# Kernel optimization log

Hardware: AMD Instinct MI355X
Metric: run time of the kernel (lower is better)

Reference implementation:

```python
import jax, jax.numpy as jnp
import numpy as np

B_SZ, L, D_MODEL = 2, 2048, 1024
EXPAND, N_STATE, K = 2, 16, 4
D_INNER = D_MODEL * EXPAND


def setup_inputs() -> dict:
    key = jax.random.key(0)
    ks = jax.random.split(key, 12)
    s = lambda k, shape, scale=0.02: jax.random.normal(k, shape, jnp.float32) * scale
    return {
        "x": jax.random.normal(ks[0], (B_SZ, L, D_MODEL), jnp.float32),
        "ln_gamma": jnp.ones((D_MODEL,), jnp.float32),
        "ln_beta": jnp.zeros((D_MODEL,), jnp.float32),
        "W_in": s(ks[1], (D_MODEL, 2 * D_INNER)),
        "conv_w": s(ks[2], (D_INNER, 1, K), 0.1),
        "conv_b": jnp.zeros((D_INNER,), jnp.float32),
        "A_log": jax.random.normal(ks[3], (N_STATE,), jnp.float32),
        "B_mat": s(ks[4], (N_STATE, D_INNER), 0.05),
        "C_mat": s(ks[5], (D_INNER, N_STATE), 0.05),
        "D_vec": s(ks[6], (D_INNER,), 0.1),
        "Wd": s(ks[7], (D_INNER, D_INNER)),
        "bd": jnp.zeros((D_INNER,), jnp.float32),
        "W_out": s(ks[8], (D_INNER, D_MODEL)),
    }


def _layernorm(x, g, b, eps=1e-5):
    mu = jnp.mean(x, axis=-1, keepdims=True)
    var = jnp.var(x, axis=-1, keepdims=True)
    return (x - mu) * jax.lax.rsqrt(var + eps) * g + b


def _selective_scan(x, delta, A, B_mat, C_mat, D_vec):
    # x: (b,l,d), delta: (b,l), A: (n,)
    dA = jnp.exp(delta[..., None] * A)            # (b,l,n)
    Bx = jnp.einsum('bld,nd->bln', x, B_mat) * delta[..., None]  # (b,l,n)

    def step(h, inp):
        dA_t, Bx_t = inp
        h = dA_t * h + Bx_t
        return h, h

    h0 = jnp.zeros((x.shape[0], A.shape[0]), x.dtype)
    # scan over seq axis
    _, hs = jax.lax.scan(step, h0, (jnp.swapaxes(dA, 0, 1), jnp.swapaxes(Bx, 0, 1)))
    hs = jnp.swapaxes(hs, 0, 1)                   # (b,l,n)
    return jnp.einsum('bln,dn->bld', hs, C_mat) + D_vec * x


def reference(x, ln_gamma, ln_beta, W_in, conv_w, conv_b, A_log, B_mat, C_mat, D_vec, Wd, bd, W_out):
    residual = x
    h = _layernorm(x, ln_gamma, ln_beta)
    xg = h @ W_in                                  # (b,l,2*d_inner)
    xs, gate = jnp.split(xg, 2, axis=-1)
    # depthwise causal conv (torch pads K-1 both sides then slices [:L] == left pad K-1)
    xc = jnp.swapaxes(xs, 1, 2)                    # (b,d,l)
    xc = jax.lax.conv_general_dilated(
        xc, conv_w, window_strides=(1,), padding=((K - 1, 0),),
        dimension_numbers=('NCH', 'OIH', 'NCH'), feature_group_count=D_INNER)
    xc = xc + conv_b[None, :, None]
    xs = jnp.swapaxes(xc, 1, 2)                    # (b,l,d)
    xs = jax.nn.silu(xs)
    # S4 kernel
    delta = jnp.mean(jax.nn.softplus(xs @ Wd + bd), axis=-1)  # (b,l)
    A = -jnp.exp(A_log)
    y = _selective_scan(xs, delta, A, B_mat, C_mat, D_vec)
    y = y * jax.nn.silu(gate)
    y = y @ W_out
    return residual + y
```

## Files before the change

kernel.cpp:

```cpp
#include <hip/hip_runtime.h>
#include <cstdint>
#include <cstddef>

typedef unsigned short u16;
typedef __attribute__((ext_vector_type(4))) float floatx4;
typedef __attribute__((ext_vector_type(8))) __bf16 bf16x8;

__device__ __forceinline__ float u2f(u16 u) {
    union { unsigned int i; float f; } x;
    x.i = ((unsigned int)u) << 16;
    return x.f;
}
__device__ __forceinline__ u16 f2u(float f) {
    union { float f; unsigned int i; } x;
    x.f = f;
    unsigned int r = x.i + 0x7fffu + ((x.i >> 16) & 1u);
    return (u16)(r >> 16);
}

__device__ __forceinline__ void swz(int bid, int& x, int& y) {
    int xcd = bid & 7;
    int lid = bid >> 3;
    x = lid >> 2;
    y = xcd * 4 + (lid & 3);
}

__device__ __forceinline__ void tr_tile(const float* __restrict__ in, u16* __restrict__ out,
                                        int K, int N, int bx, int by, float* tile ) {
    int n0 = bx * 32, k0 = by * 32;
    int t = threadIdx.x;
    int r = t >> 3, c4 = (t & 7) * 4;
    float4 v = *(const float4*)(in + (size_t)(k0 + r) * N + n0 + c4);
    tile[r * 33 + c4 + 0] = v.x;
    tile[r * 33 + c4 + 1] = v.y;
    tile[r * 33 + c4 + 2] = v.z;
    tile[r * 33 + c4 + 3] = v.w;
    __syncthreads();
    int n = t >> 3, kg = (t & 7) * 4;
    ushort4 o;
    o.x = f2u(tile[(kg + 0) * 33 + n]);
    o.y = f2u(tile[(kg + 1) * 33 + n]);
    o.z = f2u(tile[(kg + 2) * 33 + n]);
    o.w = f2u(tile[(kg + 3) * 33 + n]);
    *(ushort4*)(out + (size_t)(n0 + n) * K + k0 + kg) = o;
}

__global__ __launch_bounds__(256)
void prep_kernel(const float* __restrict__ W_in, u16* __restrict__ Wt_in,
                 const float* __restrict__ Wd, u16* __restrict__ Wt_ext,
                 const float* __restrict__ W_out, u16* __restrict__ Wt_out,
                 const float* __restrict__ B_mat,
                 const float* __restrict__ x, const float* __restrict__ gamma,
                 const float* __restrict__ beta, u16* __restrict__ h,
                 float* __restrict__ out) {
    __shared__ float tile[32 * 33];
    int blk = blockIdx.x, t = threadIdx.x;
    if (blk < 4096) {
        tr_tile(W_in, Wt_in, 1024, 4096, blk & 127, blk >> 7, tile);
    } else if (blk < 8192) {
        int b2 = blk - 4096;
        tr_tile(Wd, Wt_ext, 2048, 2048, b2 & 63, b2 >> 6, tile);
    } else if (blk < 10240) {
        int b3 = blk - 8192;
        tr_tile(W_out, Wt_out, 2048, 1024, b3 & 31, b3 >> 5, tile);
    } else if (blk < 14336) {
        int r = blk - 10240;
        const float4* xr = (const float4*)(x + (size_t)r * 1024);
        float4 xv = xr[t];
        ((float4*)(out + (size_t)r * 1024))[t] = xv;
        float s = xv.x + xv.y + xv.z + xv.w;
        float ss = xv.x * xv.x + xv.y * xv.y + xv.z * xv.z + xv.w * xv.w;
#pragma unroll
        for (int off = 32; off > 0; off >>= 1) {
            s += __shfl_down(s, off, 64);
            ss += __shfl_down(ss, off, 64);
        }
        __shared__ float rs[4], rss[4], mu_s, ri_s;
        int wave = t >> 6, lane = t & 63;
        if (lane == 0) { rs[wave] = s; rss[wave] = ss; }
        __syncthreads();
        if (t == 0) {
            float S = rs[0] + rs[1] + rs[2] + rs[3];
            float SS = rss[0] + rss[1] + rss[2] + rss[3];
            float mu = S * (1.f / 1024.f);
            float var = SS * (1.f / 1024.f) - mu * mu;
            mu_s = mu;
            ri_s = rsqrtf(fmaxf(var, 0.f) + 1e-5f);
        }
        __syncthreads();
        float mu = mu_s, ri = ri_s;
        float4 gv = ((const float4*)gamma)[t];
        float4 bv = ((const float4*)beta)[t];
        ushort4 o;
        o.x = f2u((xv.x - mu) * ri * gv.x + bv.x);
        o.y = f2u((xv.y - mu) * ri * gv.y + bv.y);
        o.z = f2u((xv.z - mu) * ri * gv.z + bv.z);
        o.w = f2u((xv.w - mu) * ri * gv.w + bv.w);
        ((ushort4*)(h + (size_t)r * 1024))[t] = o;
    } else {
        int idx = (blk - 14336) * 256 + t;
        int row = 2048 + (idx >> 11), col = idx & 2047;
        u16 v = (row < 2064) ? f2u(B_mat[(size_t)(row - 2048) * 2048 + col]) : (u16)0;
        Wt_ext[(size_t)row * 2048 + col] = v;
    }
}

__device__ __forceinline__ void gl_lds16(const u16* g, u16* l) {
    __builtin_amdgcn_global_load_lds(
        (const __attribute__((address_space(1))) void*)g,
        (__attribute__((address_space(3))) void*)l, 16, 0, 0);
}

template <int CB, int NB>
__device__ __forceinline__
void ktile256(u16 (&As)[2][16384], u16 (&Bs)[2][16384],
              const u16* __restrict__ gA, const u16* __restrict__ gB,
              int kt, bool doStage, int K,
              int w, int wr, int wc, int l16, int q,
              floatx4 (&acc)[8][4]) {
    asm volatile("s_waitcnt vmcnt(0)" ::: "memory");
    __builtin_amdgcn_s_barrier();
    asm volatile("" ::: "memory");
    bf16x8 af[4][2], bfr[4][2];
    const int aBase = wr * 128, bBase = wc * 64;
#pragma unroll
    for (int i = 0; i < 4; ++i)
#pragma unroll
        for (int h = 0; h < 2; ++h)
            af[i][h] = *(const bf16x8*)&As[CB][h * 8192 + (aBase + i * 16 + l16) * 32 + q * 8];
#pragma unroll
    for (int j = 0; j < 2; ++j)
#pragma unroll
        for (int h = 0; h < 2; ++h)
            bfr[j][h] = *(const bf16x8*)&Bs[CB][h * 8192 + (bBase + j * 16 + l16) * 32 + q * 8];
    if (doStage) {
        const u16* p = gA + (size_t)(kt + 1) * 64;
#pragma unroll
        for (int h = 0; h < 2; ++h) {
            gl_lds16(p + h * 32,                  &As[NB][h * 8192 + w * 1024]);
            gl_lds16(p + (size_t)16 * K + h * 32, &As[NB][h * 8192 + w * 1024 + 512]);
        }
    }
    __builtin_amdgcn_s_barrier();
    __builtin_amdgcn_s_setprio(1);
#pragma unroll
    for (int i = 0; i < 4; ++i)
#pragma unroll
        for (int j = 0; j < 2; ++j)
#pragma unroll
            for (int h = 0; h < 2; ++h)
                acc[i][j] = __builtin_amdgcn_mfma_f32_16x16x32_bf16(af[i][h], bfr[j][h], acc[i][j], 0, 0, 0);
    __builtin_amdgcn_s_setprio(0);
    __builtin_amdgcn_s_barrier();
#pragma unroll
    for (int j = 2; j < 4; ++j)
#pragma unroll
        for (int h = 0; h < 2; ++h)
            bfr[j][h] = *(const bf16x8*)&Bs[CB][h * 8192 + (bBase + j * 16 + l16) * 32 + q * 8];
    if (doStage) {
        const u16* p = gB + (size_t)(kt + 1) * 64;
#pragma unroll
        for (int h = 0; h < 2; ++h) {
            gl_lds16(p + h * 32,                  &Bs[NB][h * 8192 + w * 1024]);
            gl_lds16(p + (size_t)16 * K + h * 32, &Bs[NB][h * 8192 + w * 1024 + 512]);
        }
    }
    __builtin_amdgcn_s_barrier();
    __builtin_amdgcn_s_setprio(1);
#pragma unroll
    for (int i = 0; i < 4; ++i)
#pragma unroll
        for (int j = 2; j < 4; ++j)
#pragma unroll
            for (int h = 0; h < 2; ++h)
                acc[i][j] = __builtin_amdgcn_mfma_f32_16x16x32_bf16(af[i][h], bfr[j][h], acc[i][j], 0, 0, 0);
    __builtin_amdgcn_s_setprio(0);
    __builtin_amdgcn_s_barrier();
#pragma unroll
    for (int i = 0; i < 4; ++i)
#pragma unroll
        for (int h = 0; h < 2; ++h)
            af[i][h] = *(const bf16x8*)&As[CB][h * 8192 + (aBase + (4 + i) * 16 + l16) * 32 + q * 8];
    __builtin_amdgcn_s_barrier();
    __builtin_amdgcn_s_setprio(1);
#pragma unroll
    for (int i = 0; i < 4; ++i)
#pragma unroll
        for (int j = 0; j < 2; ++j)
#pragma unroll
            for (int h = 0; h < 2; ++h)
                acc[4 + i][j] = __builtin_amdgcn_mfma_f32_16x16x32_bf16(af[i][h], bfr[j][h], acc[4 + i][j], 0, 0, 0);
    __builtin_amdgcn_s_setprio(0);
    __builtin_amdgcn_s_barrier();
    __builtin_amdgcn_s_setprio(1);
#pragma unroll
    for (int i = 0; i < 4; ++i)
#pragma unroll
        for (int j = 2; j < 4; ++j)
#pragma unroll
            for (int h = 0; h < 2; ++h)
                acc[4 + i][j] = __builtin_amdgcn_mfma_f32_16x16x32_bf16(af[i][h], bfr[j][h], acc[4 + i][j], 0, 0, 0);
    __builtin_amdgcn_s_setprio(0);
    __builtin_amdgcn_s_barrier();
}

__global__ __launch_bounds__(512, 2)
void gemm_xg256(const u16* __restrict__ A, const u16* __restrict__ Bt,
                u16* __restrict__ out, int M, int N, int K) {
    __shared__ u16 As[2][16384];
    __shared__ u16 Bs[2][16384];
    const int bid = blockIdx.x;
    const int xcd = bid & 7, lid = bid >> 3;
    const int by = xcd * 2 + (lid & 1), bx = lid >> 1;
    const int tid = threadIdx.x;
    const int w = tid >> 6, lane = tid & 63;
    const int wr = w >> 2, wc = w & 3;
    const int row0 = by * 256, col0 = bx * 256;
    const int l16 = lane & 15, q = lane >> 4;
    const int sRow = lane >> 2, sK = (lane & 3) * 8;

    floatx4 acc[8][4];
#pragma unroll
    for (int i = 0; i < 8; ++i)
#pragma unroll
        for (int j = 0; j < 4; ++j) acc[i][j] = (floatx4){0.f, 0.f, 0.f, 0.f};

    const u16* gA = A + (size_t)(row0 + w * 32 + sRow) * K + sK;
    const u16* gB = Bt + (size_t)(col0 + w * 32 + sRow) * K + sK;

#pragma unroll
    for (int h = 0; h < 2; ++h) {
        gl_lds16(gA + h * 32,                  &As[0][h * 8192 + w * 1024]);
        gl_lds16(gA + (size_t)16 * K + h * 32, &As[0][h * 8192 + w * 1024 + 512]);
        gl_lds16(gB + h * 32,                  &Bs[0][h * 8192 + w * 1024]);
        gl_lds16(gB + (size_t)16 * K + h * 32, &Bs[0][h * 8192 + w * 1024 + 512]);
    }

    const int nkt = K >> 6;
    for (int t2 = 0; t2 < nkt; t2 += 2) {
        ktile256<0, 1>(As, Bs, gA, gB, t2, true, K, w, wr, wc, l16, q, acc);
        ktile256<1, 0>(As, Bs, gA, gB, t2 + 1, (t2 + 2) < nkt, K, w, wr, wc, l16, q, acc);
    }

    const int mB = row0 + wr * 128;
    const int nB = col0 + wc * 64 + l16;
#pragma unroll
    for (int mi = 0; mi < 8; ++mi)
#pragma unroll
        for (int ni = 0; ni < 4; ++ni)
#pragma unroll
            for (int rr = 0; rr < 4; ++rr)
                out[(size_t)(mB + mi * 16 + q * 4 + rr) * N + nB + ni * 16] =
                    f2u(acc[mi][ni][rr]);
}

template <int EPI>
__device__ __forceinline__
void gemm128_body(const u16* __restrict__ A, const u16* __restrict__ Bt,
                  void* __restrict__ out, int M, int N, int K, int Ksub) {
    __shared__ u16 As[128 * 64];
    __shared__ u16 Bs[128 * 64];
    int bx, by;
    swz(blockIdx.x, bx, by);
    const int tid = threadIdx.x;
    const int wave = tid >> 6, lane = tid & 63;
    const int row0 = by * 128, col0 = bx * 128;
    const int koff = blockIdx.y * Ksub;
    const int l16 = lane & 15, q = lane >> 4;
    const int sRow = lane >> 2, sK = (lane & 3) * 8;

    floatx4 acc[4][4];
#pragma unroll
    for (int i = 0; i < 4; ++i)
#pragma unroll
        for (int j = 0; j < 4; ++j) acc[i][j] = (floatx4){0.f, 0.f, 0.f, 0.f};

    const u16* gA = A + (size_t)(row0 + wave * 32 + sRow) * K + koff + sK;
    const u16* gB = Bt + (size_t)(col0 + wave * 32 + sRow) * K + koff + sK;
    u16* lA = As + wave * 1024;
    u16* lB = Bs + wave * 1024;
    const int rowb = (wave >> 1) * 64, colb = (wave & 1) * 64;

    for (int k0 = 0; k0 < Ksub; k0 += 64) {
#pragma unroll
        for (int h = 0; h < 2; ++h) {
            gl_lds16(gA + h * 32, lA + h * 4096);
            gl_lds16(gA + (size_t)16 * K + h * 32, lA + h * 4096 + 512);
            gl_lds16(gB + h * 32, lB + h * 4096);
            gl_lds16(gB + (size_t)16 * K + h * 32, lB + h * 4096 + 512);
        }
        gA += 64; gB += 64;
        __syncthreads();
#pragma unroll
        for (int h = 0; h < 2; ++h) {
            bf16x8 af[4], bfr[4];
#pragma unroll
            for (int mi = 0; mi < 4; ++mi)
                af[mi] = *(const bf16x8*)(As + h * 4096 + (rowb + mi * 16 + l16) * 32 + q * 8);
#pragma unroll
            for (int ni = 0; ni < 4; ++ni)
                bfr[ni] = *(const bf16x8*)(Bs + h * 4096 + (colb + ni * 16 + l16) * 32 + q * 8);
#pragma unroll
            for (int mi = 0; mi < 4; ++mi)
#pragma unroll
                for (int ni = 0; ni < 4; ++ni)
                    acc[mi][ni] = __builtin_amdgcn_mfma_f32_16x16x32_bf16(
                        af[mi], bfr[ni], acc[mi][ni], 0, 0, 0);
        }
        __syncthreads();
    }

    const int mB = row0 + rowb;
    const int nB = col0 + colb + l16;
    if constexpr (EPI == 0) {
        u16* o = (u16*)out;
#pragma unroll
        for (int mi = 0; mi < 4; ++mi)
#pragma unroll
            for (int ni = 0; ni < 4; ++ni)
#pragma unroll
                for (int rr = 0; rr < 4; ++rr)
                    o[(size_t)(mB + mi * 16 + q * 4 + rr) * N + nB + ni * 16] =
                        f2u(acc[mi][ni][rr]);
    } else {
        float* C = (float*)out;
#pragma unroll
        for (int mi = 0; mi < 4; ++mi)
#pragma unroll
            for (int ni = 0; ni < 4; ++ni)
#pragma unroll
                for (int rr = 0; rr < 4; ++rr)
                    atomicAdd(&C[(size_t)(mB + mi * 16 + q * 4 + rr) * N + nB + ni * 16],
                              acc[mi][ni][rr]);
    }
}

__global__ __launch_bounds__(256)
void gemm_fin(const u16* __restrict__ A, const u16* __restrict__ Bt,
              void* __restrict__ out, int M, int N, int K, int Ksub) {
    gemm128_body<4>(A, Bt, out, M, N, K, Ksub);
}

__global__ __launch_bounds__(256)
void gemm_fin_pl(const u16* __restrict__ A, const u16* __restrict__ Bt,
                 u16* __restrict__ planes, int M, int N, int K, int Ksub) {
    u16* plane = planes + (size_t)blockIdx.y * M * N;
    gemm128_body<0>(A, Bt, plane, M, N, K, Ksub);
}

__global__ __launch_bounds__(256)
void fin_reduce(const u16* __restrict__ planes, float* __restrict__ out) {
    const size_t PL = (size_t)4096 * 1024;
    const size_t idx = ((size_t)blockIdx.x * 256 + threadIdx.x) * 8;
    float acc[8] = {0.f, 0.f, 0.f, 0.f, 0.f, 0.f, 0.f, 0.f};
#pragma unroll
    for (int p = 0; p < 4; ++p) {
        ushort4 v0 = *(const ushort4*)(planes + p * PL + idx);
        ushort4 v1 = *(const ushort4*)(planes + p * PL + idx + 4);
        acc[0] += u2f(v0.x); acc[1] += u2f(v0.y); acc[2] += u2f(v0.z); acc[3] += u2f(v0.w);
        acc[4] += u2f(v1.x); acc[5] += u2f(v1.y); acc[6] += u2f(v1.z); acc[7] += u2f(v1.w);
    }
    float4 o0 = *(const float4*)(out + idx);
    float4 o1 = *(const float4*)(out + idx + 4);
    o0.x += acc[0]; o0.y += acc[1]; o0.z += acc[2]; o0.w += acc[3];
    o1.x += acc[4]; o1.y += acc[5]; o1.z += acc[6]; o1.w += acc[7];
    *(float4*)(out + idx) = o0;
    *(float4*)(out + idx + 4) = o1;
}

__global__ __launch_bounds__(256)
void gemm_delta_sk(const u16* __restrict__ A, const u16* __restrict__ Bt,
                   u16* __restrict__ planes, int M, int N, int K, int Ksub) {
    u16* plane = planes + (size_t)blockIdx.y * M * N;
    gemm128_body<0>(A, Bt, plane, M, N, K, Ksub);
}

__global__ __launch_bounds__(256)
void delta_reduce(const u16* __restrict__ planes, const float* __restrict__ bias,
                  float* __restrict__ dacc, float* __restrict__ Bdotn) {
    const int r = blockIdx.x;
    const int t = threadIdx.x;
    const size_t PL = (size_t)4096 * 2176;
    const u16* p0 = planes + (size_t)r * 2176 + t * 8;
    const u16* p1 = p0 + PL;
    ushort4 a0 = *(const ushort4*)p0;
    ushort4 a1 = *(const ushort4*)(p0 + 4);
    ushort4 b0 = *(const ushort4*)p1;
    ushort4 b1 = *(const ushort4*)(p1 + 4);
    float4 c0 = *(const float4*)(bias + t * 8);
    float4 c1 = *(const float4*)(bias + t * 8 + 4);
    float e[8];
    e[0] = u2f(a0.x) + u2f(b0.x) + c0.x;
    e[1] = u2f(a0.y) + u2f(b0.y) + c0.y;
    e[2] = u2f(a0.z) + u2f(b0.z) + c0.z;
    e[3] = u2f(a0.w) + u2f(b0.w) + c0.w;
    e[4] = u2f(a1.x) + u2f(b1.x) + c1.x;
    e[5] = u2f(a1.y) + u2f(b1.y) + c1.y;
    e[6] = u2f(a1.z) + u2f(b1.z) + c1.z;
    e[7] = u2f(a1.w) + u2f(b1.w) + c1.w;
    float sv = 0.f;
#pragma unroll
    for (int i = 0; i < 8; ++i)
        sv += (e[i] > 20.f) ? e[i] : log1pf(expf(e[i]));
#pragma unroll
    for (int off = 32; off > 0; off >>= 1)
        sv += __shfl_down(sv, off, 64);
    __shared__ float wsum[4];
    const int wave = t >> 6, lane = t & 63;
    if (lane == 0) wsum[wave] = sv;
    __syncthreads();
    if (t == 0) dacc[r] = wsum[0] + wsum[1] + wsum[2] + wsum[3];
    if (t < 16) {
        const u16* qp = planes + (size_t)r * 2176 + 2048 + t;
        Bdotn[(size_t)t * 4096 + r] = u2f(*qp) + u2f(*(qp + PL));
    }
}

__global__ __launch_bounds__(256)
void gemm_delta(const u16* __restrict__ A, const u16* __restrict__ Bt,
                float* __restrict__ dacc, const float* __restrict__ bias,
                float* __restrict__ Bdotn, int M, int N, int K) {
    __shared__ u16 As[128 * 128];
    __shared__ u16 Bs[64 * 128];
    int bx, by;
    swz(blockIdx.x, bx, by);
    const int tid = threadIdx.x;
    const int wave = tid >> 6, lane = tid & 63;
    const int row0 = by * 128, col0 = bx * 64;
    const int l16 = lane & 15, q = lane >> 4;
    const int sRow = lane >> 2, sK = (lane & 3) * 8;

    floatx4 acc[2][4];
#pragma unroll
    for (int i = 0; i < 2; ++i)
#pragma unroll
        for (int j = 0; j < 4; ++j) acc[i][j] = (floatx4){0.f, 0.f, 0.f, 0.f};

    const u16* gA = A + (size_t)(row0 + wave * 32 + sRow) * K + sK;
    const u16* gB = Bt + (size_t)(col0 + wave * 16 + sRow) * K + sK;
    u16* lA = As + wave * 1024;
    u16* lB = Bs + wave * 512;
    const int rowb = wave * 32;

    for (int k0 = 0; k0 < K; k0 += 128) {
#pragma unroll
        for (int h = 0; h < 4; ++h) {
            gl_lds16(gA + h * 32, lA + h * 4096);
            gl_lds16(gA + (size_t)16 * K + h * 32, lA + h * 4096 + 512);
            gl_lds16(gB + h * 32, lB + h * 2048);
        }
        gA += 128; gB += 128;
        __syncthreads();
#pragma unroll
        for (int h = 0; h < 4; ++h) {
            bf16x8 af[2], bfr[4];
#pragma unroll
            for (int mi = 0; mi < 2; ++mi)
                af[mi] = *(const bf16x8*)(As + h * 4096 + (rowb + mi * 16 + l16) * 32 + q * 8);
#pragma unroll
            for (int ni = 0; ni < 4; ++ni)
                bfr[ni] = *(const bf16x8*)(Bs + h * 2048 + (ni * 16 + l16) * 32 + q * 8);
#pragma unroll
            for (int mi = 0; mi < 2; ++mi)
#pragma unroll
                for (int ni = 0; ni < 4; ++ni)
                    acc[mi][ni] = __builtin_amdgcn_mfma_f32_16x16x32_bf16(
                        af[mi], bfr[ni], acc[mi][ni], 0, 0, 0);
        }
        __syncthreads();
    }

    const int mB = row0 + rowb;
    const int nB = col0 + l16;
    if (col0 < 2048) {
#pragma unroll
        for (int mi = 0; mi < 2; ++mi) {
#pragma unroll
            for (int rr = 0; rr < 4; ++rr) {
                float sv = 0.f;
#pragma unroll
                for (int ni = 0; ni < 4; ++ni) {
                    float t2 = acc[mi][ni][rr] + bias[nB + ni * 16];
                    sv += (t2 > 20.f) ? t2 : log1pf(expf(t2));
                }
#pragma unroll
                for (int off = 1; off < 16; off <<= 1)
                    sv += __shfl_xor(sv, off, 64);
                if (l16 == 0)
                    atomicAdd(&dacc[mB + mi * 16 + q * 4 + rr], sv);
            }
        }
    } else {
#pragma unroll
        for (int mi = 0; mi < 2; ++mi)
#pragma unroll
            for (int rr = 0; rr < 4; ++rr)
                Bdotn[(size_t)l16 * 4096 + mB + mi * 16 + q * 4 + rr] =
                    acc[mi][0][rr];
    }
}

__global__ __launch_bounds__(256) void conv_silu_kernel(const u16* __restrict__ xg,
                                                        const float* __restrict__ conv_w,
                                                        const float* __restrict__ conv_b,
                                                        u16* __restrict__ xsc,
                                                        float* __restrict__ delta_acc) {
    int r0 = blockIdx.x * 4;
    int l0 = r0 & 2047, bb = r0 >> 11;
    int t = threadIdx.x, d8 = t * 8;
    if (t < 4) delta_acc[r0 + t] = 0.f;

    ushort4 rw[7][2];
#pragma unroll
    for (int j = 0; j < 7; ++j) {
        int ls = l0 + j - 3;
        if (ls >= 0) {
            const u16* row = xg + (size_t)((bb << 11) + ls) * 4096 + d8;
            rw[j][0] = *(const ushort4*)row;
            rw[j][1] = *(const ushort4*)(row + 4);
        } else {
            rw[j][0] = (ushort4){0, 0, 0, 0};
            rw[j][1] = (ushort4){0, 0, 0, 0};
        }
    }
    float w[8][4];
#pragma unroll
    for (int j = 0; j < 8; ++j) {
        float4 wv = *(const float4*)(conv_w + (size_t)(d8 + j) * 4);
        w[j][0] = wv.x; w[j][1] = wv.y; w[j][2] = wv.z; w[j][3] = wv.w;
    }
    float cb[8];
    {
        float4 b0 = *(const float4*)(conv_b + d8);
        float4 b1 = *(const float4*)(conv_b + d8 + 4);
        cb[0] = b0.x; cb[1] = b0.y; cb[2] = b0.z; cb[3] = b0.w;
        cb[4] = b1.x; cb[5] = b1.y; cb[6] = b1.z; cb[7] = b1.w;
    }
#pragma unroll
    for (int i = 0; i < 4; ++i) {
        float xs[8];
#pragma unroll
        for (int j = 0; j < 8; ++j) xs[j] = cb[j];
#pragma unroll
        for (int k = 0; k < 4; ++k) {
            ushort4 u0 = rw[i + k][0], u1 = rw[i + k][1];
            xs[0] += w[0][k] * u2f(u0.x); xs[1] += w[1][k] * u2f(u0.y);
            xs[2] += w[2][k] * u2f(u0.z); xs[3] += w[3][k] * u2f(u0.w);
            xs[4] += w[4][k] * u2f(u1.x); xs[5] += w[5][k] * u2f(u1.y);
            xs[6] += w[6][k] * u2f(u1.z); xs[7] += w[7][k] * u2f(u1.w);
        }
        ushort4 o0, o1;
        o0.x = f2u(xs[0] / (1.f + expf(-xs[0])));
        o0.y = f2u(xs[1] / (1.f + expf(-xs[1])));
        o0.z = f2u(xs[2] / (1.f + expf(-xs[2])));
        o0.w = f2u(xs[3] / (1.f + expf(-xs[3])));
        o1.x = f2u(xs[4] / (1.f + expf(-xs[4])));
        o1.y = f2u(xs[5] / (1.f + expf(-xs[5])));
        o1.z = f2u(xs[6] / (1.f + expf(-xs[6])));
        o1.w = f2u(xs[7] / (1.f + expf(-xs[7])));
        u16* orow = xsc + (size_t)(r0 + i) * 2048 + d8;
        *(ushort4*)orow = o0;
        *(ushort4*)(orow + 4) = o1;
    }
}

__global__ __launch_bounds__(256) void scan_kernel(const float* __restrict__ delta_acc,
                                                   const float* __restrict__ Bdotn,
                                                   const float* __restrict__ A_log,
                                                   float* __restrict__ hsn) {
    int chain = blockIdx.x;
    int b = chain >> 4, n = chain & 15;
    int t = threadIdx.x;
    int wave = t >> 6, lane = t & 63;
    __shared__ float sd[2048], sb[2048];
    __shared__ float wA[4], wB[4];
#pragma unroll
    for (int m = 0; m < 2; ++m) {
        int idx = (m * 256 + t) * 4;
        *(float4*)(sd + idx) = *(const float4*)(delta_acc + b * 2048 + idx);
        *(float4*)(sb + idx) = *(const float4*)(Bdotn + (size_t)n * 4096 + b * 2048 + idx);
    }
    __syncthreads();
    float An = -expf(A_log[n]);
    int base = t * 8;
    float a[8], bb[8];
#pragma unroll
    for (int i = 0; i < 8; ++i) {
        float dl = sd[base + i] * (1.f / 2048.f);
        a[i] = expf(dl * An);
        bb[i] = sb[base + i] * dl;
    }
    float Aacc = 1.f, Bacc = 0.f;
#pragma unroll
    for (int i = 0; i < 8; ++i) {
        Bacc = a[i] * Bacc + bb[i];
        Aacc = a[i] * Aacc;
    }
#pragma unroll
    for (int d = 1; d < 64; d <<= 1) {
        float Ap = __shfl_up(Aacc, d, 64);
        float Bp = __shfl_up(Bacc, d, 64);
        if (lane >= d) {
            Bacc = Aacc * Bp + Bacc;
            Aacc = Aacc * Ap;
        }
    }
    if (lane == 63) { wA[wave] = Aacc; wB[wave] = Bacc; }
    float eA = __shfl_up(Aacc, 1, 64);
    float eB = __shfl_up(Bacc, 1, 64);
    if (lane == 0) { eA = 1.f; eB = 0.f; }
    __syncthreads();
    float pB = 0.f;
#pragma unroll
    for (int w = 0; w < 3; ++w)
        if (w < wave) pB = wA[w] * pB + wB[w];
    float h = eA * pB + eB;
#pragma unroll
    for (int i = 0; i < 8; ++i) {
        h = a[i] * h + bb[i];
        sd[base + i] = h;
    }
    __syncthreads();
#pragma unroll
    for (int m = 0; m < 2; ++m) {
        int idx = (m * 256 + t) * 4;
        *(float4*)(hsn + (size_t)n * 4096 + b * 2048 + idx) = *(const float4*)(sd + idx);
    }
}

__global__ __launch_bounds__(256) void ymid_kernel(const float* __restrict__ hsn,
                                                   const float* __restrict__ C_mat,
                                                   const float* __restrict__ D_vec,
                                                   const u16* __restrict__ xsc,
                                                   const u16* __restrict__ xg,
                                                   u16* __restrict__ ymid) {
    const int t = threadIdx.x;
    const int d0 = blockIdx.x * 512 + t * 2;
    const int r0 = blockIdx.y * 16;
    __shared__ float hsv[16 * 16];
    {
        int rl = t >> 4, nn = t & 15;
        hsv[t] = hsn[(size_t)nn * 4096 + r0 + rl];
    }
    float c0[16], c1[16];
#pragma unroll
    for (int k = 0; k < 4; ++k) {
        float4 v0 = *(const float4*)(C_mat + (size_t)d0 * 16 + k * 4);
        float4 v1 = *(const float4*)(C_mat + (size_t)(d0 + 1) * 16 + k * 4);
        c0[k * 4 + 0] = v0.x; c0[k * 4 + 1] = v0.y; c0[k * 4 + 2] = v0.z; c0[k * 4 + 3] = v0.w;
        c1[k * 4 + 0] = v1.x; c1[k * 4 + 1] = v1.y; c1[k * 4 + 2] = v1.z; c1[k * 4 + 3] = v1.w;
    }
    const float dv0 = D_vec[d0], dv1 = D_vec[d0 + 1];
    __syncthreads();
#pragma unroll 4
    for (int rl = 0; rl < 16; ++rl) {
        const int r = r0 + rl;
        float h0 = 0.f, h1 = 0.f;
#pragma unroll
        for (int nn = 0; nn < 16; ++nn) {
            float hv = hsv[rl * 16 + nn];
            h0 += hv * c0[nn];
            h1 += hv * c1[nn];
        }
        unsigned int xv = *(const unsigned int*)(xsc + (size_t)r * 2048 + d0);
        unsigned int gv = *(const unsigned int*)(xg + (size_t)r * 4096 + 2048 + d0);
        float x0 = u2f((u16)(xv & 0xffffu)), x1 = u2f((u16)(xv >> 16));
        float g0 = u2f((u16)(gv & 0xffffu)), g1 = u2f((u16)(gv >> 16));
        float y0 = (h0 + dv0 * x0) * (g0 / (1.f + expf(-g0)));
        float y1 = (h1 + dv1 * x1) * (g1 / (1.f + expf(-g1)));
        unsigned int o = (unsigned int)f2u(y0) | ((unsigned int)f2u(y1) << 16);
        *(unsigned int*)(ymid + (size_t)r * 2048 + d0) = o;
    }
}

extern "C" void kernel_launch(void* const* d_in, const int* in_sizes, int n_in,
                              void* d_out, int out_size, void* d_ws, size_t ws_size,
                              hipStream_t stream) {
    (void)in_sizes; (void)n_in;
    const float* x      = (const float*)d_in[0];
    const float* ln_g   = (const float*)d_in[1];
    const float* ln_b   = (const float*)d_in[2];
    const float* W_in   = (const float*)d_in[3];
    const float* conv_w = (const float*)d_in[4];
    const float* conv_b = (const float*)d_in[5];
    const float* A_log  = (const float*)d_in[6];
    const float* B_mat  = (const float*)d_in[7];
    const float* C_mat  = (const float*)d_in[8];
    const float* D_vec  = (const float*)d_in[9];
    const float* Wd     = (const float*)d_in[10];
    const float* bd     = (const float*)d_in[11];
    const float* W_out  = (const float*)d_in[12];
    float* out = (float*)d_out;

    char* base = (char*)d_ws;
    u16* Wt_in  = (u16*)base;
    u16* h_ln   = (u16*)base + 4096ull * 1024;
    u16* ymid   = (u16*)base;
    u16* Wt_ext = (u16*)(base + (16ull << 20));
    u16* Wt_out = (u16*)(base + (25ull << 20));
    u16* xg     = (u16*)(base + (29ull << 20));
    u16* xsc    = (u16*)(base + (61ull << 20));
    float* delta_acc = (float*)(base + (77ull << 20));
    float* Bdotn = delta_acc + 4096;
    float* hsn   = Bdotn + 16 * 4096;
    u16* planes  = (u16*)(base + (78ull << 20));
    u16* fplanes = (u16*)(base + (78ull << 20));
    size_t needed = (77ull << 20) + 4096ull * 4 * (1 + 2 * 16);
    size_t needed_sk = (78ull << 20) + 2ull * 4096 * 2176 * 2;

    if (needed > ws_size) {
        hipMemsetAsync(d_out, 0x7F, (size_t)out_size * 4, stream);
        return;
    }
    const bool use_sk = (ws_size >= needed_sk);

    prep_kernel<<<14848, 256, 0, stream>>>(W_in, Wt_in, Wd, Wt_ext, W_out, Wt_out,
                                           B_mat, x, ln_g, ln_b, h_ln, out);
    gemm_xg256<<<256, 512, 0, stream>>>(h_ln, Wt_in, xg, 4096, 4096, 1024);
    conv_silu_kernel<<<1024, 256, 0, stream>>>(xg, conv_w, conv_b, xsc, delta_acc);
    if (use_sk) {
        gemm_delta_sk<<<dim3(544, 2), 256, 0, stream>>>(xsc, Wt_ext, planes,
                                                        4096, 2176, 2048, 1024);
        delta_reduce<<<4096, 256, 0, stream>>>(planes, bd, delta_acc, Bdotn);
    } else {
        gemm_delta<<<1056, 256, 0, stream>>>(xsc, Wt_ext, delta_acc, bd, Bdotn,
                                             4096, 2112, 2048);
    }
    scan_kernel<<<32, 256, 0, stream>>>(delta_acc, Bdotn, A_log, hsn);
    ymid_kernel<<<dim3(4, 256), 256, 0, stream>>>(hsn, C_mat, D_vec, xsc, xg, ymid);
    if (use_sk) {
        gemm_fin_pl<<<dim3(256, 4), 256, 0, stream>>>(ymid, Wt_out, fplanes,
                                                      4096, 1024, 2048, 512);
        fin_reduce<<<2048, 256, 0, stream>>>(fplanes, out);
    } else {
        gemm_fin<<<dim3(256, 2), 256, 0, stream>>>(ymid, Wt_out, out, 4096, 1024, 2048, 1024);
    }
}
```

Baseline: 314.2 us.

## Add XOR-swizzled LDS layout and reuse 256-tile GEMM for split-K output projection

Adds an XOR swizzle to the k-chunk offset used both for global-to-LDS staging and for the LDS fragment reads of the 256x256 GEMM, aiming to cut LDS bank conflicts. The 256-tile body is generalized with a k offset and k length so the final output-projection split-K GEMM can use it in place of the 128-tile kernel, with fewer, larger blocks of 512 threads. The larger tiles raise data reuse per block, but the final GEMM then launches only 256 blocks, which may underfill the GPU.

```diff
diff --git a/kernel.cpp b/kernel.cpp
--- a/kernel.cpp
+++ b/kernel.cpp
@@ -116,7 +116,7 @@
 void ktile256(u16 (&As)[2][16384], u16 (&Bs)[2][16384],
               const u16* __restrict__ gA, const u16* __restrict__ gB,
               int kt, bool doStage, int K,
-              int w, int wr, int wc, int l16, int q,
+              int w, int wr, int wc, int l16, int qsw,
               floatx4 (&acc)[8][4]) {
     asm volatile("s_waitcnt vmcnt(0)" ::: "memory");
     __builtin_amdgcn_s_barrier();
@@ -127,12 +127,12 @@
     for (int i = 0; i < 4; ++i)
 #pragma unroll
         for (int h = 0; h < 2; ++h)
-            af[i][h] = *(const bf16x8*)&As[CB][h * 8192 + (aBase + i * 16 + l16) * 32 + q * 8];
+            af[i][h] = *(const bf16x8*)&As[CB][h * 8192 + (aBase + i * 16 + l16) * 32 + qsw * 8];
 #pragma unroll
     for (int j = 0; j < 2; ++j)
 #pragma unroll
         for (int h = 0; h < 2; ++h)
-            bfr[j][h] = *(const bf16x8*)&Bs[CB][h * 8192 + (bBase + j * 16 + l16) * 32 + q * 8];
+            bfr[j][h] = *(const bf16x8*)&Bs[CB][h * 8192 + (bBase + j * 16 + l16) * 32 + qsw * 8];
     if (doStage) {
         const u16* p = gA + (size_t)(kt + 1) * 64;
 #pragma unroll
@@ -156,7 +156,7 @@
     for (int j = 2; j < 4; ++j)
 #pragma unroll
         for (int h = 0; h < 2; ++h)
-            bfr[j][h] = *(const bf16x8*)&Bs[CB][h * 8192 + (bBase + j * 16 + l16) * 32 + q * 8];
+            bfr[j][h] = *(const bf16x8*)&Bs[CB][h * 8192 + (bBase + j * 16 + l16) * 32 + qsw * 8];
     if (doStage) {
         const u16* p = gB + (size_t)(kt + 1) * 64;
 #pragma unroll
@@ -180,7 +180,7 @@
     for (int i = 0; i < 4; ++i)
 #pragma unroll
         for (int h = 0; h < 2; ++h)
-            af[i][h] = *(const bf16x8*)&As[CB][h * 8192 + (aBase + (4 + i) * 16 + l16) * 32 + q * 8];
+            af[i][h] = *(const bf16x8*)&As[CB][h * 8192 + (aBase + (4 + i) * 16 + l16) * 32 + qsw * 8];
     __builtin_amdgcn_s_barrier();
     __builtin_amdgcn_s_setprio(1);
 #pragma unroll
@@ -204,20 +204,20 @@
     __builtin_amdgcn_s_barrier();
 }
 
-__global__ __launch_bounds__(512, 2)
-void gemm_xg256(const u16* __restrict__ A, const u16* __restrict__ Bt,
-                u16* __restrict__ out, int M, int N, int K) {
+__device__ __forceinline__
+void gemm256_body(const u16* __restrict__ A, const u16* __restrict__ Bt,
+                  u16* __restrict__ out, int M, int N, int K,
+                  int koff, int Ksub, int bx, int by) {
     __shared__ u16 As[2][16384];
     __shared__ u16 Bs[2][16384];
-    const int bid = blockIdx.x;
-    const int xcd = bid & 7, lid = bid >> 3;
-    const int by = xcd * 2 + (lid & 1), bx = lid >> 1;
     const int tid = threadIdx.x;
     const int w = tid >> 6, lane = tid & 63;
     const int wr = w >> 2, wc = w & 3;
     const int row0 = by * 256, col0 = bx * 256;
     const int l16 = lane & 15, q = lane >> 4;
-    const int sRow = lane >> 2, sK = (lane & 3) * 8;
+    const int sRow = lane >> 2;
+    const int sKsw = ((lane & 3) ^ ((lane >> 4) & 3)) * 8;
+    const int qsw = q ^ ((l16 >> 2) & 3);
 
     floatx4 acc[8][4];
 #pragma unroll
@@ -225,8 +225,8 @@
 #pragma unroll
         for (int j = 0; j < 4; ++j) acc[i][j] = (floatx4){0.f, 0.f, 0.f, 0.f};
 
-    const u16* gA = A + (size_t)(row0 + w * 32 + sRow) * K + sK;
-    const u16* gB = Bt + (size_t)(col0 + w * 32 + sRow) * K + sK;
+    const u16* gA = A + (size_t)(row0 + w * 32 + sRow) * K + koff + sKsw;
+    const u16* gB = Bt + (size_t)(col0 + w * 32 + sRow) * K + koff + sKsw;
 
 #pragma unroll
     for (int h = 0; h < 2; ++h) {
@@ -236,10 +236,10 @@
         gl_lds16(gB + (size_t)16 * K + h * 32, &Bs[0][h * 8192 + w * 1024 + 512]);
     }
 
-    const int nkt = K >> 6;
+    const int nkt = Ksub >> 6;
     for (int t2 = 0; t2 < nkt; t2 += 2) {
-        ktile256<0, 1>(As, Bs, gA, gB, t2, true, K, w, wr, wc, l16, q, acc);
-        ktile256<1, 0>(As, Bs, gA, gB, t2 + 1, (t2 + 2) < nkt, K, w, wr, wc, l16, q, acc);
+        ktile256<0, 1>(As, Bs, gA, gB, t2, true, K, w, wr, wc, l16, qsw, acc);
+        ktile256<1, 0>(As, Bs, gA, gB, t2 + 1, (t2 + 2) < nkt, K, w, wr, wc, l16, qsw, acc);
     }
 
     const int mB = row0 + wr * 128;
@@ -252,6 +252,24 @@
             for (int rr = 0; rr < 4; ++rr)
                 out[(size_t)(mB + mi * 16 + q * 4 + rr) * N + nB + ni * 16] =
                     f2u(acc[mi][ni][rr]);
+}
+
+__global__ __launch_bounds__(512, 2)
+void gemm_xg256(const u16* __restrict__ A, const u16* __restrict__ Bt,
+                u16* __restrict__ out, int M, int N, int K) {
+    const int bid = blockIdx.x;
+    const int xcd = bid & 7, lid = bid >> 3;
+    const int by = xcd * 2 + (lid & 1), bx = lid >> 1;
+    gemm256_body(A, Bt, out, M, N, K, 0, K, bx, by);
+}
+
+__global__ __launch_bounds__(512, 2)
+void gemm_fin256(const u16* __restrict__ A, const u16* __restrict__ Bt,
+                 u16* __restrict__ planes, int M, int N, int K, int Ksub) {
+    u16* plane = planes + (size_t)blockIdx.y * M * N;
+    const int bid = blockIdx.x;
+    const int bx = bid >> 4, by = bid & 15;
+    gemm256_body(A, Bt, plane, M, N, K, blockIdx.y * Ksub, Ksub, bx, by);
 }
 
 template <int EPI>
@@ -339,13 +357,6 @@
 void gemm_fin(const u16* __restrict__ A, const u16* __restrict__ Bt,
               void* __restrict__ out, int M, int N, int K, int Ksub) {
     gemm128_body<4>(A, Bt, out, M, N, K, Ksub);
-}
-
-__global__ __launch_bounds__(256)
-void gemm_fin_pl(const u16* __restrict__ A, const u16* __restrict__ Bt,
-                 u16* __restrict__ planes, int M, int N, int K, int Ksub) {
-    u16* plane = planes + (size_t)blockIdx.y * M * N;
-    gemm128_body<0>(A, Bt, plane, M, N, K, Ksub);
 }
 
 __global__ __launch_bounds__(256)
@@ -729,8 +740,8 @@
     scan_kernel<<<32, 256, 0, stream>>>(delta_acc, Bdotn, A_log, hsn);
     ymid_kernel<<<dim3(4, 256), 256, 0, stream>>>(hsn, C_mat, D_vec, xsc, xg, ymid);
     if (use_sk) {
-        gemm_fin_pl<<<dim3(256, 4), 256, 0, stream>>>(ymid, Wt_out, fplanes,
-                                                      4096, 1024, 2048, 512);
+        gemm_fin256<<<dim3(64, 4), 512, 0, stream>>>(ymid, Wt_out, fplanes,
+                                                     4096, 1024, 2048, 512);
         fin_reduce<<<2048, 256, 0, stream>>>(fplanes, out);
     } else {
         gemm_fin<<<dim3(256, 2), 256, 0, stream>>>(ymid, Wt_out, out, 4096, 1024, 2048, 1024);
```

After: 314.9 us. About the same (+0.2%).
